# Performance work log

Hardware: AMD Instinct MI355X
Metric: run time of the kernel (lower is better)

Reference implementation:

```python
import jax, jax.numpy as jnp
import numpy as np

M0, M1 = 16, 16          # n_modes
C = 64                   # hidden_channels
B = 16                   # batch
H = W = 128              # spatial resolution
SCALE = C ** (-2)        # matches torch: scale * torch.rand(...)


def setup_inputs() -> dict:
    key = jax.random.key(0)
    kx, k0r, k0i, k1r, k1i = jax.random.split(key, 5)
    X = jax.random.normal(kx, (B, C, H, W), dtype=jnp.float32)
    wshape = (C, C, M0, M1)
    # torch.rand with cfloat draws U[0,1) for real and imag parts independently
    w0r = SCALE * jax.random.uniform(k0r, wshape, dtype=jnp.float32)
    w0i = SCALE * jax.random.uniform(k0i, wshape, dtype=jnp.float32)
    w1r = SCALE * jax.random.uniform(k1r, wshape, dtype=jnp.float32)
    w1i = SCALE * jax.random.uniform(k1i, wshape, dtype=jnp.float32)
    return {"X": X, "w0r": w0r, "w0i": w0i, "w1r": w1r, "w1i": w1i}


def reference(X, w0r, w0i, w1r, w1i):
    w0 = w0r + 1j * w0i                       # linear0: (C, C, M0, M1) complex
    w1 = w1r + 1j * w1i                       # linear1
    Xf = jnp.fft.rfftn(X, axes=(-2, -1), norm="forward")   # (B, C, H, W//2+1) complex
    # out[b,c] = sum_t weight[c,t] * Xf[b,t] on the two kept-mode corners
    top = jnp.einsum("ctxy,btxy->bcxy", w0, Xf[:, :, :M0, :M1])
    bot = jnp.einsum("ctxy,btxy->bcxy", w1, Xf[:, :, -M0:, :M1])
    Y = jnp.zeros_like(Xf)
    Y = Y.at[:, :, :M0, :M1].set(top)
    Y = Y.at[:, :, -M0:, :M1].set(bot)
    out = jnp.fft.irfftn(Y, axes=(-2, -1), s=(H, W), norm="forward")
    return out.astype(jnp.float32)
```

## Files before the change

### kernel.cpp

```cpp
#include <hip/hip_runtime.h>

#define PI2 6.28318530717958647692f

__global__ __launch_bounds__(256) void k_fwd(const float* __restrict__ X,
                                             float* __restrict__ Xf) {
  __shared__ __attribute__((aligned(16))) float E1t[64 * 32 * 2];
  __shared__ __attribute__((aligned(16))) float A2t[128 * 34 * 2];
  __shared__ __attribute__((aligned(16))) float E2t[64 * 16 * 2];
  const int plane = blockIdx.x;
  const int tid = threadIdx.x;
  const float* Xp = X + (size_t)plane * (128 * 128);

  #pragma unroll
  for (int k = 0; k < 8; ++k) {
    int idx = tid + k * 256;
    int h = idx >> 5, kxi = idx & 31;
    int kx = kxi + ((kxi >> 4) ? 96 : 0);
    float ang = -PI2 * (float)((kx * h) & 127) / 128.f;
    float s_, c_;
    __sincosf(ang, &s_, &c_);
    E1t[idx * 2] = c_; E1t[idx * 2 + 1] = s_;
  }
  #pragma unroll
  for (int k = 0; k < 4; ++k) {
    int idx = tid + k * 256;
    int w = idx >> 4, ky = idx & 15;
    float ang = -PI2 * (float)((ky * w) & 127) / 128.f;
    float s_, c_;
    __sincosf(ang, &s_, &c_);
    E2t[idx * 2] = c_; E2t[idx * 2 + 1] = s_;
  }
  __syncthreads();

  {
    const int w = tid & 127;
    const int kxg = tid >> 7;
    float cr[16], ci[16];
    #pragma unroll
    for (int j = 0; j < 16; ++j) { cr[j] = 0.f; ci[j] = 0.f; }
    float x0 = Xp[w], x1 = Xp[64 * 128 + w];
    for (int h = 0; h < 64; ++h) {
      float nx0 = 0.f, nx1 = 0.f;
      if (h < 63) { nx0 = Xp[(h + 1) * 128 + w]; nx1 = Xp[(h + 65) * 128 + w]; }
      float ue = x0 + x1;
      float uo = x0 - x1;
      const float4* Erow = (const float4*)&E1t[(h * 32 + kxg * 16) * 2];
      #pragma unroll
      for (int j2 = 0; j2 < 8; ++j2) {
        float4 e = Erow[j2];
        cr[2 * j2]     = fmaf(ue, e.x, cr[2 * j2]);
        ci[2 * j2]     = fmaf(ue, e.y, ci[2 * j2]);
        cr[2 * j2 + 1] = fmaf(uo, e.z, cr[2 * j2 + 1]);
        ci[2 * j2 + 1] = fmaf(uo, e.w, ci[2 * j2 + 1]);
      }
      x0 = nx0; x1 = nx1;
    }
    #pragma unroll
    for (int j = 0; j < 16; ++j) {
      int f2i = w * 34 + kxg * 16 + j;
      A2t[f2i * 2] = cr[j]; A2t[f2i * 2 + 1] = ci[j];
    }
  }
  __syncthreads();

  {
    const int kxi = tid >> 3;
    const int t = tid & 7;
    const float s = (t & 1) ? -1.f : 1.f;
    float r0 = 0.f, i0 = 0.f, r1 = 0.f, i1 = 0.f;
    for (int w = 0; w < 64; ++w) {
      const float2 a = *(const float2*)&A2t[(w * 34 + kxi) * 2];
      const float2 b = *(const float2*)&A2t[((w + 64) * 34 + kxi) * 2];
      float ur = fmaf(s, b.x, a.x);
      float ui = fmaf(s, b.y, a.y);
      const float2 e0 = *(const float2*)&E2t[(w * 16 + t) * 2];
      const float2 e1 = *(const float2*)&E2t[(w * 16 + t + 8) * 2];
      r0 = fmaf(ur, e0.x, r0); r0 = fmaf(-ui, e0.y, r0);
      i0 = fmaf(ur, e0.y, i0); i0 = fmaf(ui, e0.x, i0);
      r1 = fmaf(ur, e1.x, r1); r1 = fmaf(-ui, e1.y, r1);
      i1 = fmaf(ur, e1.y, i1); i1 = fmaf(ui, e1.x, i1);
    }
    const float sc = 1.f / 16384.f;
    float* base = Xf + (size_t)plane * 1024 + kxi * 32;
    *(float2*)&base[t * 2]       = make_float2(r0 * sc, i0 * sc);
    *(float2*)&base[(t + 8) * 2] = make_float2(r1 * sc, i1 * sc);
  }
}

__global__ __launch_bounds__(256) void k_mix(const float* __restrict__ Xf,
                                             const float* __restrict__ w0r,
                                             const float* __restrict__ w0i,
                                             const float* __restrict__ w1r,
                                             const float* __restrict__ w1i,
                                             float* __restrict__ Y) {
  __shared__ __attribute__((aligned(16))) float Wl[4 * 64 * 16 * 2];
  const int bid = blockIdx.x;
  const int c2 = bid >> 8;
  const int x  = (bid >> 4) & 15;
  const int cg = bid & 15;
  const int c0 = cg * 4;
  const int kxi = c2 * 16 + x;
  const float* Wr_g = c2 ? w1r : w0r;
  const float* Wi_g = c2 ? w1i : w0i;
  const int tid = threadIdx.x;
  const int b = tid >> 4;
  const int y = tid & 15;

  #pragma unroll
  for (int k = 0; k < 16; ++k) {
    int idx = tid + k * 256;
    int y_ = idx & 15, t_ = (idx >> 4) & 63, c_ = idx >> 10;
    size_t ga = (((size_t)(c0 + c_) * 64 + t_) * 16 + x) * 16 + y_;
    float wr = Wr_g[ga], wi = Wi_g[ga];
    Wl[idx * 2] = wr; Wl[idx * 2 + 1] = wi;
  }
  __syncthreads();

  float aR[4] = {}, aI[4] = {};
  const float* xbase = Xf + ((size_t)b * 64) * 1024 + kxi * 32 + y * 2;
  for (int t4 = 0; t4 < 64; t4 += 4) {
    float2 xv[4];
    #pragma unroll
    for (int q = 0; q < 4; ++q)
      xv[q] = *(const float2*)&xbase[(size_t)(t4 + q) * 1024];
    #pragma unroll
    for (int q = 0; q < 4; ++q) {
      int t = t4 + q;
      #pragma unroll
      for (int cj = 0; cj < 4; ++cj) {
        const float2 wv = *(const float2*)&Wl[((cj * 64 + t) * 16 + y) * 2];
        aR[cj] = fmaf(xv[q].x, wv.x, aR[cj]);
        aR[cj] = fmaf(-xv[q].y, wv.y, aR[cj]);
        aI[cj] = fmaf(xv[q].x, wv.y, aI[cj]);
        aI[cj] = fmaf(xv[q].y, wv.x, aI[cj]);
      }
    }
  }
  #pragma unroll
  for (int cj = 0; cj < 4; ++cj) {
    size_t ya = ((size_t)(b * 64 + c0 + cj)) * 1024 + kxi * 32 + y * 2;
    *(float2*)&Y[ya] = make_float2(aR[cj], aI[cj]);
  }
}

__global__ __launch_bounds__(256) void k_inv(const float* __restrict__ Y,
                                             float* __restrict__ out) {
  __shared__ __attribute__((aligned(16))) float Yl[1024];
  __shared__ __attribute__((aligned(16))) float Ml[128 * 18 * 2];
  const int plane = blockIdx.x;
  const int tid = threadIdx.x;
  {
    *(float4*)&Yl[tid * 4] = *(const float4*)&Y[(size_t)plane * 1024 + tid * 4];
  }
  __syncthreads();

  {
    const int g = tid >> 7;
    const int h = tid & 127;
    float zr[8] = {}, zi[8] = {};
    float uw, uwi;
    __sincosf(PI2 * (float)h / 128.f, &uwi, &uw);
    const float4* Yl4 = (const float4*)Yl;
    float Tr = 1.f, Ti = 0.f;
    #pragma unroll 4
    for (int kxi = 0; kxi < 16; ++kxi) {
      #pragma unroll
      for (int q = 0; q < 4; ++q) {
        float4 p = Yl4[kxi * 8 + g * 4 + q];
        int m = 2 * q;
        zr[m]   = fmaf(p.x, Tr, zr[m]);   zr[m]   = fmaf(-p.y, Ti, zr[m]);
        zi[m]   = fmaf(p.x, Ti, zi[m]);   zi[m]   = fmaf(p.y, Tr, zi[m]);
        zr[m+1] = fmaf(p.z, Tr, zr[m+1]); zr[m+1] = fmaf(-p.w, Ti, zr[m+1]);
        zi[m+1] = fmaf(p.z, Ti, zi[m+1]); zi[m+1] = fmaf(p.w, Tr, zi[m+1]);
      }
      float nr = Tr * uw - Ti * uwi, ni = Tr * uwi + Ti * uw;
      Tr = nr; Ti = ni;
    }
    __sincosf(PI2 * (float)((112 * h) & 127) / 128.f, &Ti, &Tr);
    #pragma unroll 4
    for (int kxi = 16; kxi < 32; ++kxi) {
      #pragma unroll
      for (int q = 0; q < 4; ++q) {
        float4 p = Yl4[kxi * 8 + g * 4 + q];
        int m = 2 * q;
        zr[m]   = fmaf(p.x, Tr, zr[m]);   zr[m]   = fmaf(-p.y, Ti, zr[m]);
        zi[m]   = fmaf(p.x, Ti, zi[m]);   zi[m]   = fmaf(p.y, Tr, zi[m]);
        zr[m+1] = fmaf(p.z, Tr, zr[m+1]); zr[m+1] = fmaf(-p.w, Ti, zr[m+1]);
        zi[m+1] = fmaf(p.z, Ti, zi[m+1]); zi[m+1] = fmaf(p.w, Tr, zi[m+1]);
      }
      float nr = Tr * uw - Ti * uwi, ni = Tr * uwi + Ti * uw;
      Tr = nr; Ti = ni;
    }
    #pragma unroll
    for (int m = 0; m < 8; ++m) {
      int ky = g * 8 + m;
      float f = (ky == 0) ? 1.f : 2.f;
      int f2i = h * 18 + ky;
      Ml[f2i * 2]     =  f * zr[m];
      Ml[f2i * 2 + 1] = -f * zi[m];
    }
  }
  __syncthreads();

  {
    const int hq = tid >> 6;
    const int w = tid & 63;
    float C[16], S[16];
    {
      float cw, sw;
      __sincosf(PI2 * (float)w / 128.f, &sw, &cw);
      C[0] = 1.f; S[0] = 0.f;
      #pragma unroll
      for (int k = 1; k < 16; ++k) {
        C[k] = C[k - 1] * cw - S[k - 1] * sw;
        S[k] = C[k - 1] * sw + S[k - 1] * cw;
      }
    }
    float* op = out + (size_t)plane * (128 * 128);
    const float4* Ml4 = (const float4*)Ml;
    for (int hj = 0; hj < 32; ++hj) {
      int h = hq * 32 + hj;
      float e = 0.f, o = 0.f;
      #pragma unroll
      for (int j2 = 0; j2 < 8; ++j2) {
        float4 m01 = Ml4[h * 9 + j2];
        int k = 2 * j2;
        float t0 = m01.x * C[k] + m01.y * S[k];
        float t1 = m01.z * C[k + 1] + m01.w * S[k + 1];
        e += t0; o += t1;
      }
      op[h * 128 + w]      = e + o;
      op[h * 128 + w + 64] = e - o;
    }
  }
}

extern "C" void kernel_launch(void* const* d_in, const int* in_sizes, int n_in,
                              void* d_out, int out_size, void* d_ws, size_t ws_size,
                              hipStream_t stream) {
  const float* X   = (const float*)d_in[0];
  const float* w0r = (const float*)d_in[1];
  const float* w0i = (const float*)d_in[2];
  const float* w1r = (const float*)d_in[3];
  const float* w1i = (const float*)d_in[4];
  float* outp = (float*)d_out;
  float* Xf = (float*)d_ws;
  float* Yw = (float*)d_ws + (1u << 20);
  k_fwd<<<1024, 256, 0, stream>>>(X, Xf);
  k_mix<<<512, 256, 0, stream>>>(Xf, w0r, w0i, w1r, w1i, Yw);
  k_inv<<<1024, 256, 0, stream>>>(Yw, outp);
}
```

Baseline: 183.4 us.

## Shrink shared memory via conjugate-symmetric twiddles and XOR swizzle, split mix blocks

The forward kernel now uses a single 16-entry twiddle table for the column DFT. It derives the high-frequency rows (kx=112..127) as conjugates of the low ones, reuses the same LDS buffer for the row twiddles, and stores the intermediate with an XOR swizzle instead of padding. The mix kernel handles two output channels per block with twice as many blocks. The inverse kernel transposes its intermediate to a ky-major layout. All three kernels add a launch-bounds minimum of 4 blocks per CU, aiming to cut LDS and register footprint for higher occupancy, at the cost of branch divergence and extra register pressure.

```diff
diff --git a/kernel.cpp b/kernel.cpp
--- a/kernel.cpp
+++ b/kernel.cpp
@@ -2,64 +2,89 @@
 
 #define PI2 6.28318530717958647692f
 
-__global__ __launch_bounds__(256) void k_fwd(const float* __restrict__ X,
-                                             float* __restrict__ Xf) {
-  __shared__ __attribute__((aligned(16))) float E1t[64 * 32 * 2];
-  __shared__ __attribute__((aligned(16))) float A2t[128 * 34 * 2];
-  __shared__ __attribute__((aligned(16))) float E2t[64 * 16 * 2];
+__global__ __launch_bounds__(256, 4) void k_fwd(const float* __restrict__ X,
+                                                float* __restrict__ Xf) {
+  __shared__ __attribute__((aligned(16))) float A2t[128 * 32 * 2];
+  __shared__ __attribute__((aligned(16))) float Tt[64 * 16 * 2];
   const int plane = blockIdx.x;
   const int tid = threadIdx.x;
   const float* Xp = X + (size_t)plane * (128 * 128);
 
   #pragma unroll
-  for (int k = 0; k < 8; ++k) {
+  for (int k = 0; k < 4; ++k) {
     int idx = tid + k * 256;
-    int h = idx >> 5, kxi = idx & 31;
-    int kx = kxi + ((kxi >> 4) ? 96 : 0);
+    int h = idx >> 4, kx = (idx & 15) + 1;
     float ang = -PI2 * (float)((kx * h) & 127) / 128.f;
     float s_, c_;
     __sincosf(ang, &s_, &c_);
-    E1t[idx * 2] = c_; E1t[idx * 2 + 1] = s_;
-  }
+    Tt[idx * 2] = c_; Tt[idx * 2 + 1] = s_;
+  }
+  __syncthreads();
+
+  {
+    const int w = tid & 127;
+    const int kxg = tid >> 7;
+    const int swz = w & 30;
+    float cr[16], ci[16];
+    #pragma unroll
+    for (int j = 0; j < 16; ++j) { cr[j] = 0.f; ci[j] = 0.f; }
+    float x0 = Xp[w], x1 = Xp[64 * 128 + w];
+    if (kxg == 0) {
+      for (int h = 0; h < 64; ++h) {
+        float nx0 = 0.f, nx1 = 0.f;
+        if (h < 63) { nx0 = Xp[(h + 1) * 128 + w]; nx1 = Xp[(h + 65) * 128 + w]; }
+        float ue = x0 + x1, uo = x0 - x1;
+        const float4* Trow = (const float4*)&Tt[h * 32];
+        cr[0] += ue;
+        #pragma unroll
+        for (int m = 0; m < 7; ++m) {
+          float4 e = Trow[m];
+          cr[2 * m + 1] = fmaf(uo, e.x, cr[2 * m + 1]);
+          ci[2 * m + 1] = fmaf(uo, e.y, ci[2 * m + 1]);
+          cr[2 * m + 2] = fmaf(ue, e.z, cr[2 * m + 2]);
+          ci[2 * m + 2] = fmaf(ue, e.w, ci[2 * m + 2]);
+        }
+        { float4 e = Trow[7];
+          cr[15] = fmaf(uo, e.x, cr[15]);
+          ci[15] = fmaf(uo, e.y, ci[15]); }
+        x0 = nx0; x1 = nx1;
+      }
+    } else {
+      for (int h = 0; h < 64; ++h) {
+        float nx0 = 0.f, nx1 = 0.f;
+        if (h < 63) { nx0 = Xp[(h + 1) * 128 + w]; nx1 = Xp[(h + 65) * 128 + w]; }
+        float ue = x0 + x1, uo = x0 - x1;
+        const float4* Trow = (const float4*)&Tt[h * 32];
+        #pragma unroll
+        for (int m = 0; m < 7; ++m) {
+          float4 e = Trow[m];
+          cr[15 - 2 * m] = fmaf(uo, e.x, cr[15 - 2 * m]);
+          ci[15 - 2 * m] = fmaf(-uo, e.y, ci[15 - 2 * m]);
+          cr[14 - 2 * m] = fmaf(ue, e.z, cr[14 - 2 * m]);
+          ci[14 - 2 * m] = fmaf(-ue, e.w, ci[14 - 2 * m]);
+        }
+        { float4 e = Trow[7];
+          cr[1] = fmaf(uo, e.x, cr[1]); ci[1] = fmaf(-uo, e.y, ci[1]);
+          cr[0] = fmaf(ue, e.z, cr[0]); ci[0] = fmaf(-ue, e.w, ci[0]); }
+        x0 = nx0; x1 = nx1;
+      }
+    }
+    #pragma unroll
+    for (int j = 0; j < 16; ++j) {
+      int f2i = w * 32 + ((kxg * 16 + j) ^ swz);
+      *(float2*)&A2t[f2i * 2] = make_float2(cr[j], ci[j]);
+    }
+  }
+  __syncthreads();
+
   #pragma unroll
   for (int k = 0; k < 4; ++k) {
     int idx = tid + k * 256;
-    int w = idx >> 4, ky = idx & 15;
-    float ang = -PI2 * (float)((ky * w) & 127) / 128.f;
+    int w_ = idx >> 4, ky = idx & 15;
+    float ang = -PI2 * (float)((ky * w_) & 127) / 128.f;
     float s_, c_;
     __sincosf(ang, &s_, &c_);
-    E2t[idx * 2] = c_; E2t[idx * 2 + 1] = s_;
-  }
-  __syncthreads();
-
-  {
-    const int w = tid & 127;
-    const int kxg = tid >> 7;
-    float cr[16], ci[16];
-    #pragma unroll
-    for (int j = 0; j < 16; ++j) { cr[j] = 0.f; ci[j] = 0.f; }
-    float x0 = Xp[w], x1 = Xp[64 * 128 + w];
-    for (int h = 0; h < 64; ++h) {
-      float nx0 = 0.f, nx1 = 0.f;
-      if (h < 63) { nx0 = Xp[(h + 1) * 128 + w]; nx1 = Xp[(h + 65) * 128 + w]; }
-      float ue = x0 + x1;
-      float uo = x0 - x1;
-      const float4* Erow = (const float4*)&E1t[(h * 32 + kxg * 16) * 2];
-      #pragma unroll
-      for (int j2 = 0; j2 < 8; ++j2) {
-        float4 e = Erow[j2];
-        cr[2 * j2]     = fmaf(ue, e.x, cr[2 * j2]);
-        ci[2 * j2]     = fmaf(ue, e.y, ci[2 * j2]);
-        cr[2 * j2 + 1] = fmaf(uo, e.z, cr[2 * j2 + 1]);
-        ci[2 * j2 + 1] = fmaf(uo, e.w, ci[2 * j2 + 1]);
-      }
-      x0 = nx0; x1 = nx1;
-    }
-    #pragma unroll
-    for (int j = 0; j < 16; ++j) {
-      int f2i = w * 34 + kxg * 16 + j;
-      A2t[f2i * 2] = cr[j]; A2t[f2i * 2 + 1] = ci[j];
-    }
+    Tt[idx * 2] = c_; Tt[idx * 2 + 1] = s_;
   }
   __syncthreads();
 
@@ -69,12 +94,13 @@
     const float s = (t & 1) ? -1.f : 1.f;
     float r0 = 0.f, i0 = 0.f, r1 = 0.f, i1 = 0.f;
     for (int w = 0; w < 64; ++w) {
-      const float2 a = *(const float2*)&A2t[(w * 34 + kxi) * 2];
-      const float2 b = *(const float2*)&A2t[((w + 64) * 34 + kxi) * 2];
+      const int col = kxi ^ (w & 30);
+      const float2 a = *(const float2*)&A2t[(w * 32 + col) * 2];
+      const float2 b = *(const float2*)&A2t[((w + 64) * 32 + col) * 2];
       float ur = fmaf(s, b.x, a.x);
       float ui = fmaf(s, b.y, a.y);
-      const float2 e0 = *(const float2*)&E2t[(w * 16 + t) * 2];
-      const float2 e1 = *(const float2*)&E2t[(w * 16 + t + 8) * 2];
+      const float2 e0 = *(const float2*)&Tt[(w * 16 + t) * 2];
+      const float2 e1 = *(const float2*)&Tt[(w * 16 + t + 8) * 2];
       r0 = fmaf(ur, e0.x, r0); r0 = fmaf(-ui, e0.y, r0);
       i0 = fmaf(ur, e0.y, i0); i0 = fmaf(ui, e0.x, i0);
       r1 = fmaf(ur, e1.x, r1); r1 = fmaf(-ui, e1.y, r1);
@@ -87,18 +113,18 @@
   }
 }
 
-__global__ __launch_bounds__(256) void k_mix(const float* __restrict__ Xf,
-                                             const float* __restrict__ w0r,
-                                             const float* __restrict__ w0i,
-                                             const float* __restrict__ w1r,
-                                             const float* __restrict__ w1i,
-                                             float* __restrict__ Y) {
-  __shared__ __attribute__((aligned(16))) float Wl[4 * 64 * 16 * 2];
+__global__ __launch_bounds__(256, 4) void k_mix(const float* __restrict__ Xf,
+                                                const float* __restrict__ w0r,
+                                                const float* __restrict__ w0i,
+                                                const float* __restrict__ w1r,
+                                                const float* __restrict__ w1i,
+                                                float* __restrict__ Y) {
+  __shared__ __attribute__((aligned(16))) float Wl[2 * 64 * 16 * 2];
   const int bid = blockIdx.x;
-  const int c2 = bid >> 8;
-  const int x  = (bid >> 4) & 15;
-  const int cg = bid & 15;
-  const int c0 = cg * 4;
+  const int c2 = bid >> 9;
+  const int x  = (bid >> 5) & 15;
+  const int cg = bid & 31;
+  const int c0 = cg * 2;
   const int kxi = c2 * 16 + x;
   const float* Wr_g = c2 ? w1r : w0r;
   const float* Wi_g = c2 ? w1i : w0i;
@@ -107,7 +133,7 @@
   const int y = tid & 15;
 
   #pragma unroll
-  for (int k = 0; k < 16; ++k) {
+  for (int k = 0; k < 8; ++k) {
     int idx = tid + k * 256;
     int y_ = idx & 15, t_ = (idx >> 4) & 63, c_ = idx >> 10;
     size_t ga = (((size_t)(c0 + c_) * 64 + t_) * 16 + x) * 16 + y_;
@@ -116,7 +142,7 @@
   }
   __syncthreads();
 
-  float aR[4] = {}, aI[4] = {};
+  float aR[2] = {}, aI[2] = {};
   const float* xbase = Xf + ((size_t)b * 64) * 1024 + kxi * 32 + y * 2;
   for (int t4 = 0; t4 < 64; t4 += 4) {
     float2 xv[4];
@@ -127,7 +153,7 @@
     for (int q = 0; q < 4; ++q) {
       int t = t4 + q;
       #pragma unroll
-      for (int cj = 0; cj < 4; ++cj) {
+      for (int cj = 0; cj < 2; ++cj) {
         const float2 wv = *(const float2*)&Wl[((cj * 64 + t) * 16 + y) * 2];
         aR[cj] = fmaf(xv[q].x, wv.x, aR[cj]);
         aR[cj] = fmaf(-xv[q].y, wv.y, aR[cj]);
@@ -137,16 +163,16 @@
     }
   }
   #pragma unroll
-  for (int cj = 0; cj < 4; ++cj) {
+  for (int cj = 0; cj < 2; ++cj) {
     size_t ya = ((size_t)(b * 64 + c0 + cj)) * 1024 + kxi * 32 + y * 2;
     *(float2*)&Y[ya] = make_float2(aR[cj], aI[cj]);
   }
 }
 
-__global__ __launch_bounds__(256) void k_inv(const float* __restrict__ Y,
-                                             float* __restrict__ out) {
+__global__ __launch_bounds__(256, 4) void k_inv(const float* __restrict__ Y,
+                                                float* __restrict__ out) {
   __shared__ __attribute__((aligned(16))) float Yl[1024];
-  __shared__ __attribute__((aligned(16))) float Ml[128 * 18 * 2];
+  __shared__ __attribute__((aligned(16))) float Mt[16 * 128 * 2];
   const int plane = blockIdx.x;
   const int tid = threadIdx.x;
   {
@@ -195,9 +221,7 @@
     for (int m = 0; m < 8; ++m) {
       int ky = g * 8 + m;
       float f = (ky == 0) ? 1.f : 2.f;
-      int f2i = h * 18 + ky;
-      Ml[f2i * 2]     =  f * zr[m];
-      Ml[f2i * 2 + 1] = -f * zi[m];
+      *(float2*)&Mt[(ky * 128 + h) * 2] = make_float2(f * zr[m], -f * zi[m]);
     }
   }
   __syncthreads();
@@ -217,16 +241,17 @@
       }
     }
     float* op = out + (size_t)plane * (128 * 128);
-    const float4* Ml4 = (const float4*)Ml;
+    const float2* Mt2 = (const float2*)Mt;
     for (int hj = 0; hj < 32; ++hj) {
       int h = hq * 32 + hj;
       float e = 0.f, o = 0.f;
       #pragma unroll
       for (int j2 = 0; j2 < 8; ++j2) {
-        float4 m01 = Ml4[h * 9 + j2];
+        float2 m0 = Mt2[(2 * j2) * 128 + h];
+        float2 m1 = Mt2[(2 * j2 + 1) * 128 + h];
         int k = 2 * j2;
-        float t0 = m01.x * C[k] + m01.y * S[k];
-        float t1 = m01.z * C[k + 1] + m01.w * S[k + 1];
+        float t0 = m0.x * C[k] + m0.y * S[k];
+        float t1 = m1.x * C[k + 1] + m1.y * S[k + 1];
         e += t0; o += t1;
       }
       op[h * 128 + w]      = e + o;
@@ -247,6 +272,6 @@
   float* Xf = (float*)d_ws;
   float* Yw = (float*)d_ws + (1u << 20);
   k_fwd<<<1024, 256, 0, stream>>>(X, Xf);
-  k_mix<<<512, 256, 0, stream>>>(Xf, w0r, w0i, w1r, w1i, Yw);
+  k_mix<<<1024, 256, 0, stream>>>(Xf, w0r, w0i, w1r, w1i, Yw);
   k_inv<<<1024, 256, 0, stream>>>(Yw, outp);
 }
```

New measurement: 182.3 us. Within noise of the previous version (-0.6%).
